# Kernel optimization log

Measured on AMD Instinct MI355X. Metric: run time of the kernel, lower is better.

Reference implementation:

```python
import jax, jax.numpy as jnp
import numpy as np

N_NODES = 50000
N_EDGES = 800000
N_GRAPHS = 64
IN_DIM, HID1, HID2, N_CLASSES = 128, 256, 128, 10


def setup_inputs() -> dict:
    key = jax.random.key(0)
    ks = jax.random.split(key, 12)
    x = jax.random.normal(ks[0], (N_NODES, IN_DIM), dtype=jnp.float32)
    src = jax.random.randint(ks[1], (N_EDGES,), 0, N_NODES, dtype=jnp.int32)
    dst = jax.random.randint(ks[2], (N_EDGES,), 0, N_NODES, dtype=jnp.int32)
    graph_id = jnp.sort(jax.random.randint(ks[3], (N_NODES,), 0, N_GRAPHS, dtype=jnp.int32))
    s1 = 1.0 / np.sqrt(IN_DIM)
    s2 = 1.0 / np.sqrt(HID1)
    s3 = 1.0 / np.sqrt(HID2)
    s4 = 1.0 / np.sqrt(12)
    return {
        'x': x, 'src': src, 'dst': dst, 'graph_id': graph_id,
        'W1': jax.random.normal(ks[4], (IN_DIM, HID1), dtype=jnp.float32) * s1,
        'b1': jnp.zeros((HID1,), dtype=jnp.float32),
        'W2': jax.random.normal(ks[5], (HID1, HID2), dtype=jnp.float32) * s2,
        'b2': jnp.zeros((HID2,), dtype=jnp.float32),
        'Wc1': jax.random.normal(ks[6], (HID2, 12), dtype=jnp.float32) * s3,
        'bc1': jnp.zeros((12,), dtype=jnp.float32),
        'Wc2': jax.random.normal(ks[7], (12, 12), dtype=jnp.float32) * s4,
        'bc2': jnp.zeros((12,), dtype=jnp.float32),
        'Wc3': jax.random.normal(ks[8], (12, N_CLASSES), dtype=jnp.float32) * s4,
        'bc3': jnp.zeros((N_CLASSES,), dtype=jnp.float32),
    }


def _graph_conv(x, W, b, src, dst, inv_sqrt_out, inv_sqrt_in, n_nodes):
    # DGL GraphConv, norm='both': D_out^{-1/2} applied to source feats,
    # sum-aggregate over edges, then D_in^{-1/2} on destination, then +bias.
    # Weight applied first (equivalent by linearity; reduces gather traffic
    # when out_dim < in_dim, and is exactly what DGL does in that case).
    xw = (x * inv_sqrt_out[:, None]) @ W                      # [N, out]
    agg = jax.ops.segment_sum(xw[src], dst, num_segments=n_nodes)  # SpMM
    return agg * inv_sqrt_in[:, None] + b


def reference(x, src, dst, graph_id, W1, b1, W2, b2, Wc1, bc1, Wc2, bc2, Wc3, bc3):
    n = x.shape[0]
    ones_e = jnp.ones(src.shape, dtype=x.dtype)
    deg_out = jnp.maximum(jax.ops.segment_sum(ones_e, src, num_segments=n), 1.0)
    deg_in = jnp.maximum(jax.ops.segment_sum(ones_e, dst, num_segments=n), 1.0)
    inv_o = jax.lax.rsqrt(deg_out)
    inv_i = jax.lax.rsqrt(deg_in)

    h = jax.nn.relu(_graph_conv(x, W1, b1, src, dst, inv_o, inv_i, n))
    h = jax.nn.relu(_graph_conv(h, W2, b2, src, dst, inv_o, inv_i, n))

    # dgl.mean_nodes: per-graph mean over nodes of the batched graph
    gsum = jax.ops.segment_sum(h, graph_id, num_segments=N_GRAPHS)   # [G, HID2]
    cnt = jnp.maximum(jax.ops.segment_sum(jnp.ones((n,), dtype=h.dtype), graph_id, num_segments=N_GRAPHS), 1.0)
    hg = gsum / cnt[:, None]

    # tiny 3-layer MLP (no activations in between, as in the source)
    out = hg @ Wc1 + bc1
    out = out @ Wc2 + bc2
    out = out @ Wc3 + bc3
    return out
```

## Files before the change

### kernel.cpp

```cpp
#include <hip/hip_runtime.h>
#include <hip/hip_bf16.h>

#define IN_DIM 128
#define HID1 256
#define HID2 128

#define HB_BINS 12500
#define HB_WORDS 6250
#define HB_CHUNKS 64
__global__ __launch_bounds__(256) void hist_src(const int* __restrict__ src,
                                                int E, int chunk_size,
                                                int* __restrict__ part, int N) {
    __shared__ int sm[HB_WORDS];
    const int base = blockIdx.y * HB_BINS;
    const int ebeg = blockIdx.x * chunk_size;
    const int eend = min(ebeg + chunk_size, E);
    for (int w = threadIdx.x; w < HB_WORDS; w += 256) sm[w] = 0;
    __syncthreads();
    for (int e = ebeg + threadIdx.x; e < eend; e += 256) {
        int v = src[e] - base;
        if ((unsigned)v < (unsigned)HB_BINS)
            atomicAdd(&sm[v >> 1], 1 << ((v & 1) * 16));
    }
    __syncthreads();
    const int nb = min(HB_BINS, N - base);
    int* dp = part + (size_t)blockIdx.x * N + base;
    for (int w = threadIdx.x; 2 * w < nb; w += 256) {
        int packed = sm[w];
        int b = 2 * w;
        dp[b] = packed & 0xffff;
        if (b + 1 < nb) dp[b + 1] = (packed >> 16) & 0xffff;
    }
}

__global__ __launch_bounds__(256) void hist_src_reduce(const int* __restrict__ part,
                                                       int N, float* __restrict__ inv_o) {
    int b = blockIdx.x * blockDim.x + threadIdx.x;
    if (b >= N) return;
    int d = 0;
#pragma unroll 4
    for (int k = 0; k < HB_CHUNKS; ++k) d += part[(size_t)k * N + b];
    inv_o[b] = rsqrtf((float)max(d, 1));
}

#define BK_SHIFT 8
#define NBUCK 196
#define NCHUNK 256
__global__ __launch_bounds__(256) void coarse_hist(const int* __restrict__ dst, int E,
                                                   int chunk_size, int* __restrict__ ccnt,
                                                   float* __restrict__ hg, int hg_n) {
    __shared__ int cnt[NBUCK];
    if (blockIdx.x == 0)
        for (int i = threadIdx.x; i < hg_n; i += 256) hg[i] = 0.f;
    for (int i = threadIdx.x; i < NBUCK; i += 256) cnt[i] = 0;
    __syncthreads();
    int ebeg = blockIdx.x * chunk_size, eend = min(ebeg + chunk_size, E);
    for (int e = ebeg + threadIdx.x; e < eend; e += 256)
        atomicAdd(&cnt[dst[e] >> BK_SHIFT], 1);
    __syncthreads();
    for (int i = threadIdx.x; i < NBUCK; i += 256) ccnt[blockIdx.x * NBUCK + i] = cnt[i];
}

__global__ __launch_bounds__(NCHUNK) void coarse_col(const int* __restrict__ ccnt,
                                                     int* __restrict__ coffpre,
                                                     int* __restrict__ ctot) {
    __shared__ int sm[NCHUNK];
    const int b = blockIdx.x, t = threadIdx.x;
    int v = ccnt[t * NBUCK + b];
    sm[t] = v;
    __syncthreads();
#pragma unroll
    for (int off = 1; off < NCHUNK; off <<= 1) {
        int u = (t >= off) ? sm[t - off] : 0;
        __syncthreads();
        sm[t] += u;
        __syncthreads();
    }
    coffpre[t * NBUCK + b] = sm[t] - v;
    if (t == NCHUNK - 1) ctot[b] = sm[t];
}

__device__ __forceinline__ void scan_bbase(const int* __restrict__ ctot, int* sm, int* bbase) {
    const int t = threadIdx.x;
    int v = (t < NBUCK) ? ctot[t] : 0;
    sm[t] = v;
    __syncthreads();
#pragma unroll
    for (int off = 1; off < 256; off <<= 1) {
        int u = (t >= off) ? sm[t - off] : 0;
        __syncthreads();
        sm[t] += u;
        __syncthreads();
    }
    if (t < NBUCK) bbase[t] = sm[t] - v;
    __syncthreads();
}

__global__ __launch_bounds__(256) void scat_a(const int* __restrict__ src,
                                              const int* __restrict__ dst, int E,
                                              int chunk_size,
                                              const int* __restrict__ coffpre,
                                              const int* __restrict__ ctot,
                                              int2* __restrict__ pairs) {
    __shared__ int sm[256];
    __shared__ int bbase[NBUCK];
    __shared__ int lcur[NBUCK];
    scan_bbase(ctot, sm, bbase);
    for (int i = threadIdx.x; i < NBUCK; i += 256)
        lcur[i] = bbase[i] + coffpre[blockIdx.x * NBUCK + i];
    __syncthreads();
    int ebeg = blockIdx.x * chunk_size, eend = min(ebeg + chunk_size, E);
    for (int e = ebeg + threadIdx.x; e < eend; e += 256) {
        int d = dst[e];
        int p = atomicAdd(&lcur[d >> BK_SHIFT], 1);
        pairs[p] = make_int2(src[e], d);
    }
}

__global__ __launch_bounds__(256) void scat_b(const int2* __restrict__ pairs,
                                              const int* __restrict__ ctot, int N,
                                              int* __restrict__ row,
                                              float* __restrict__ inv_i,
                                              int* __restrict__ csr_src) {
    __shared__ int sm[256];
    __shared__ int bbase[NBUCK];
    __shared__ int cnt[1 << BK_SHIFT];
    __shared__ int cur[1 << BK_SHIFT];
    const int b = blockIdx.x, t = threadIdx.x;
    scan_bbase(ctot, sm, bbase);
    const int segBase = bbase[b];
    const int segEnd = segBase + ctot[b];
    const int nb0 = b << BK_SHIFT;
    const int nbn = min(256, N - nb0);
    cnt[t] = 0;
    __syncthreads();
    for (int j = segBase + t; j < segEnd; j += 256)
        atomicAdd(&cnt[pairs[j].y - nb0], 1);
    __syncthreads();
    int v = cnt[t];
    sm[t] = v;
    __syncthreads();
#pragma unroll
    for (int off = 1; off < 256; off <<= 1) {
        int u = (t >= off) ? sm[t - off] : 0;
        __syncthreads();
        sm[t] += u;
        __syncthreads();
    }
    int excl = sm[t] - v;
    cur[t] = segBase + excl;
    if (t < nbn) {
        row[nb0 + t] = segBase + excl;
        inv_i[nb0 + t] = rsqrtf((float)max(v, 1));
        if (nb0 + t == N - 1) row[N] = segBase + excl + v;
    }
    __syncthreads();
    for (int j = segBase + t; j < segEnd; j += 256) {
        int2 pr = pairs[j];
        int p = atomicAdd(&cur[pr.y - nb0], 1);
        csr_src[p] = pr.x;
    }
}

__global__ void cvt_all(const float* __restrict__ x, const float* __restrict__ inv_o,
                        __hip_bfloat16* __restrict__ x_bf, int n4x,
                        const float* __restrict__ W1, __hip_bfloat16* __restrict__ W1t,
                        const float* __restrict__ W2, __hip_bfloat16* __restrict__ W2t) {
    const int S1 = IN_DIM * HID1;
    const int S2 = HID1 * HID2;
    int i = blockIdx.x * blockDim.x + threadIdx.x;
    if (i < n4x) {
        float s = inv_o[i >> 5];
        float4 v = reinterpret_cast<const float4*>(x)[i];
        __hip_bfloat16 b0 = __float2bfloat16(v.x * s);
        __hip_bfloat16 b1 = __float2bfloat16(v.y * s);
        __hip_bfloat16 b2 = __float2bfloat16(v.z * s);
        __hip_bfloat16 b3 = __float2bfloat16(v.w * s);
        ushort4 o = make_ushort4(*(unsigned short*)&b0, *(unsigned short*)&b1,
                                 *(unsigned short*)&b2, *(unsigned short*)&b3);
        reinterpret_cast<ushort4*>(x_bf)[i] = o;
    } else {
        int idx = i - n4x;
        if (idx < S1) {
            int k = idx / HID1, n = idx - k * HID1;
            W1t[n * IN_DIM + k] = __float2bfloat16(W1[idx]);
        } else if (idx < S1 + S2) {
            int j = idx - S1;
            int k = j / HID2, n = j - k * HID2;
            W2t[n * HID1 + k] = __float2bfloat16(W2[j]);
        }
    }
}

__device__ __forceinline__ void bf2_unpack(unsigned int p, float& lo, float& hi) {
    lo = __uint_as_float(p << 16);
    hi = __uint_as_float(p & 0xffff0000u);
}

__global__ __launch_bounds__(256) void spmm_kernel(const __hip_bfloat16* __restrict__ feat,
                                                   const int* __restrict__ row,
                                                   const int* __restrict__ csr_src,
                                                   __hip_bfloat16* __restrict__ out_bf, int N) {
    const int node = blockIdx.x * 4 + (threadIdx.x >> 6);
    if (node >= N) return;
    const int lane = threadIdx.x & 63;
    const unsigned int* fp = (const unsigned int*)feat;
    const int beg = row[node];
    const int end = row[node + 1];
    float a0 = 0.f, a1 = 0.f;
    int j = beg;
    for (; j + 8 <= end; j += 8) {
        int s0 = csr_src[j],     s1 = csr_src[j + 1], s2 = csr_src[j + 2], s3 = csr_src[j + 3];
        int s4 = csr_src[j + 4], s5 = csr_src[j + 5], s6 = csr_src[j + 6], s7 = csr_src[j + 7];
        unsigned int p0 = fp[(size_t)s0 * 64 + lane];
        unsigned int p1 = fp[(size_t)s1 * 64 + lane];
        unsigned int p2 = fp[(size_t)s2 * 64 + lane];
        unsigned int p3 = fp[(size_t)s3 * 64 + lane];
        unsigned int p4 = fp[(size_t)s4 * 64 + lane];
        unsigned int p5 = fp[(size_t)s5 * 64 + lane];
        unsigned int p6 = fp[(size_t)s6 * 64 + lane];
        unsigned int p7 = fp[(size_t)s7 * 64 + lane];
        float lo, hi;
        bf2_unpack(p0, lo, hi); a0 += lo; a1 += hi;
        bf2_unpack(p1, lo, hi); a0 += lo; a1 += hi;
        bf2_unpack(p2, lo, hi); a0 += lo; a1 += hi;
        bf2_unpack(p3, lo, hi); a0 += lo; a1 += hi;
        bf2_unpack(p4, lo, hi); a0 += lo; a1 += hi;
        bf2_unpack(p5, lo, hi); a0 += lo; a1 += hi;
        bf2_unpack(p6, lo, hi); a0 += lo; a1 += hi;
        bf2_unpack(p7, lo, hi); a0 += lo; a1 += hi;
    }
    for (; j + 4 <= end; j += 4) {
        int s0 = csr_src[j], s1 = csr_src[j + 1], s2 = csr_src[j + 2], s3 = csr_src[j + 3];
        unsigned int p0 = fp[(size_t)s0 * 64 + lane];
        unsigned int p1 = fp[(size_t)s1 * 64 + lane];
        unsigned int p2 = fp[(size_t)s2 * 64 + lane];
        unsigned int p3 = fp[(size_t)s3 * 64 + lane];
        float lo, hi;
        bf2_unpack(p0, lo, hi); a0 += lo; a1 += hi;
        bf2_unpack(p1, lo, hi); a0 += lo; a1 += hi;
        bf2_unpack(p2, lo, hi); a0 += lo; a1 += hi;
        bf2_unpack(p3, lo, hi); a0 += lo; a1 += hi;
    }
    for (; j < end; ++j) {
        unsigned int p0 = fp[(size_t)csr_src[j] * 64 + lane];
        float lo, hi;
        bf2_unpack(p0, lo, hi); a0 += lo; a1 += hi;
    }
    __hip_bfloat16 b0 = __float2bfloat16(a0);
    __hip_bfloat16 b1 = __float2bfloat16(a1);
    unsigned int packed = (unsigned int)(*(unsigned short*)&b0) |
                          ((unsigned int)(*(unsigned short*)&b1) << 16);
    ((unsigned int*)out_bf)[(size_t)node * 64 + lane] = packed;
}

#define SP_NODES 8
__global__ __launch_bounds__(256) void spmm_pool_kernel(const __hip_bfloat16* __restrict__ feat,
                                                        const int* __restrict__ row,
                                                        const int* __restrict__ csr_src,
                                                        const float* __restrict__ inv_i,
                                                        const float* __restrict__ b2,
                                                        const int* __restrict__ graph_id,
                                                        int N, float* __restrict__ hg_sum) {
    const int wave = blockIdx.x * 4 + (threadIdx.x >> 6);
    const int lane = threadIdx.x & 63;
    const int n0 = wave * SP_NODES;
    if (n0 >= N) return;
    const int n1 = min(n0 + SP_NODES, N);
    const unsigned int* fp = (const unsigned int*)feat;
    const float bias0 = b2[2 * lane];
    const float bias1 = b2[2 * lane + 1];
    int g = graph_id[n0];
    float p0s = 0.f, p1s = 0.f;
    for (int node = n0; node < n1; ++node) {
        int gi = graph_id[node];
        if (gi != g) {
            atomicAdd(&hg_sum[g * HID2 + 2 * lane], p0s);
            atomicAdd(&hg_sum[g * HID2 + 2 * lane + 1], p1s);
            p0s = p1s = 0.f;
            g = gi;
        }
        const int beg = row[node];
        const int end = row[node + 1];
        float a0 = 0.f, a1 = 0.f;
        int j = beg;
        for (; j + 4 <= end; j += 4) {
            int s0 = csr_src[j], s1 = csr_src[j + 1], s2 = csr_src[j + 2], s3 = csr_src[j + 3];
            unsigned int q0 = fp[(size_t)s0 * 64 + lane];
            unsigned int q1 = fp[(size_t)s1 * 64 + lane];
            unsigned int q2 = fp[(size_t)s2 * 64 + lane];
            unsigned int q3 = fp[(size_t)s3 * 64 + lane];
            float lo, hi;
            bf2_unpack(q0, lo, hi); a0 += lo; a1 += hi;
            bf2_unpack(q1, lo, hi); a0 += lo; a1 += hi;
            bf2_unpack(q2, lo, hi); a0 += lo; a1 += hi;
            bf2_unpack(q3, lo, hi); a0 += lo; a1 += hi;
        }
        for (; j < end; ++j) {
            unsigned int q0 = fp[(size_t)csr_src[j] * 64 + lane];
            float lo, hi;
            bf2_unpack(q0, lo, hi); a0 += lo; a1 += hi;
        }
        float ii = inv_i[node];
        p0s += fmaxf(a0 * ii + bias0, 0.f);
        p1s += fmaxf(a1 * ii + bias1, 0.f);
    }
    atomicAdd(&hg_sum[g * HID2 + 2 * lane], p0s);
    atomicAdd(&hg_sum[g * HID2 + 2 * lane + 1], p1s);
}

#define GBM 128
#define GBN 128
#define GBK 32
#define LPAD 40
typedef __attribute__((ext_vector_type(4))) float floatx4;
typedef __attribute__((ext_vector_type(8))) short shortx8;

__global__ __launch_bounds__(256) void mfma_gemm_kernel(const __hip_bfloat16* __restrict__ A,
                                                        const __hip_bfloat16* __restrict__ Bt,
                                                        __hip_bfloat16* __restrict__ C,
                                                        const float* __restrict__ scaleR,
                                                        const float* __restrict__ bias,
                                                        const float* __restrict__ scaleO,
                                                        int M, int Nn, int K, int doRelu) {
    __shared__ __align__(16) __hip_bfloat16 As[GBM * LPAD];
    __shared__ __align__(16) __hip_bfloat16 Bs[GBN * LPAD];
    const int tid = threadIdx.x;
    const int bm = blockIdx.x * GBM;
    const int bn = blockIdx.y * GBN;
    const int wid = tid >> 6;
    const int lane = tid & 63;
    const int wm = (wid & 1) * 64;
    const int wn = (wid >> 1) * 64;
    const int lrow = lane & 15;
    const int quad = lane >> 4;

    floatx4 acc[4][4] = {};

    for (int k0 = 0; k0 < K; k0 += GBK) {
#pragma unroll
        for (int it = 0; it < 2; ++it) {
            int slot = tid + (it << 8);
            int r = slot >> 2;
            int c = (slot & 3) << 3;
            int gr = bm + r;
            float4 v = make_float4(0.f, 0.f, 0.f, 0.f);
            if (gr < M) v = *reinterpret_cast<const float4*>(A + (size_t)gr * K + k0 + c);
            *reinterpret_cast<float4*>(&As[r * LPAD + c]) = v;
        }
#pragma unroll
        for (int it = 0; it < 2; ++it) {
            int slot = tid + (it << 8);
            int r = slot >> 2;
            int c = (slot & 3) << 3;
            float4 v = *reinterpret_cast<const float4*>(Bt + (size_t)(bn + r) * K + k0 + c);
            *reinterpret_cast<float4*>(&Bs[r * LPAD + c]) = v;
        }
        __syncthreads();

        shortx8 af[4], bf[4];
#pragma unroll
        for (int i = 0; i < 4; ++i)
            af[i] = *reinterpret_cast<const shortx8*>(&As[(wm + i * 16 + lrow) * LPAD + quad * 8]);
#pragma unroll
        for (int i = 0; i < 4; ++i)
            bf[i] = *reinterpret_cast<const shortx8*>(&Bs[(wn + i * 16 + lrow) * LPAD + quad * 8]);
#pragma unroll
        for (int im = 0; im < 4; ++im)
#pragma unroll
            for (int in = 0; in < 4; ++in)
                acc[im][in] = __builtin_amdgcn_mfma_f32_16x16x32_bf16(af[im], bf[in], acc[im][in], 0, 0, 0);
        __syncthreads();
    }

    float bv[4];
#pragma unroll
    for (int in = 0; in < 4; ++in)
        bv[in] = bias ? bias[bn + wn + in * 16 + lrow] : 0.f;

#pragma unroll
    for (int im = 0; im < 4; ++im) {
#pragma unroll
        for (int reg = 0; reg < 4; ++reg) {
            int r = bm + wm + im * 16 + quad * 4 + reg;
            if (r >= M) continue;
            float sR = scaleR ? scaleR[r] : 1.f;
            float sO = scaleO ? scaleO[r] : 1.f;
#pragma unroll
            for (int in = 0; in < 4; ++in) {
                int c = bn + wn + in * 16 + lrow;
                float v = acc[im][in][reg] * sR + bv[in];
                if (doRelu) v = fmaxf(v, 0.f);
                v *= sO;
                C[(size_t)r * Nn + c] = __float2bfloat16(v);
            }
        }
    }
}

__device__ __forceinline__ int lower_bound_i(const int* a, int n, int key) {
    int lo = 0, hi = n;
    while (lo < hi) {
        int mid = (lo + hi) >> 1;
        if (a[mid] < key) lo = mid + 1; else hi = mid;
    }
    return lo;
}

__global__ __launch_bounds__(64) void mlp_kernel(const float* __restrict__ hg_sum,
                                                 const int* __restrict__ graph_id, int n,
                                                 const float* __restrict__ Wc1, const float* __restrict__ bc1,
                                                 const float* __restrict__ Wc2, const float* __restrict__ bc2,
                                                 const float* __restrict__ Wc3, const float* __restrict__ bc3,
                                                 float* __restrict__ out) {
    const int g = blockIdx.x;
    const int t = threadIdx.x;
    __shared__ float h[HID2];
    __shared__ float t1[12];
    __shared__ float t2[12];
    __shared__ float s_inv_cnt;
    if (t == 0) {
        int beg = lower_bound_i(graph_id, n, g);
        int end = lower_bound_i(graph_id, n, g + 1);
        int c = end - beg;
        s_inv_cnt = 1.0f / (float)max(c, 1);
    }
    __syncthreads();
    const float ic = s_inv_cnt;
    for (int i = t; i < HID2; i += 64) h[i] = hg_sum[g * HID2 + i] * ic;
    __syncthreads();
    if (t < 12) {
        float a = bc1[t];
        for (int k = 0; k < HID2; ++k) a += h[k] * Wc1[k * 12 + t];
        t1[t] = a;
    }
    __syncthreads();
    if (t < 12) {
        float a = bc2[t];
        for (int k = 0; k < 12; ++k) a += t1[k] * Wc2[k * 12 + t];
        t2[t] = a;
    }
    __syncthreads();
    if (t < 10) {
        float a = bc3[t];
        for (int k = 0; k < 12; ++k) a += t2[k] * Wc3[k * 10 + t];
        out[g * 10 + t] = a;
    }
}

extern "C" void kernel_launch(void* const* d_in, const int* in_sizes, int n_in,
                              void* d_out, int out_size, void* d_ws, size_t ws_size,
                              hipStream_t stream) {
    const float* x        = (const float*)d_in[0];
    const int*   src      = (const int*)d_in[1];
    const int*   dst      = (const int*)d_in[2];
    const int*   graph_id = (const int*)d_in[3];
    const float* W1       = (const float*)d_in[4];
    const float* b1       = (const float*)d_in[5];
    const float* W2       = (const float*)d_in[6];
    const float* b2       = (const float*)d_in[7];
    const float* Wc1      = (const float*)d_in[8];
    const float* bc1      = (const float*)d_in[9];
    const float* Wc2      = (const float*)d_in[10];
    const float* bc2      = (const float*)d_in[11];
    const float* Wc3      = (const float*)d_in[12];
    const float* bc3      = (const float*)d_in[13];
    float* out = (float*)d_out;

    const int N = in_sizes[0] / IN_DIM;
    const int E = in_sizes[1];
    const int G = out_size / 10;

    char* ws = (char*)d_ws;
    size_t off = 0;
    auto alloc = [&](size_t bytes) -> char* {
        char* p = ws + off;
        off = (off + bytes + 255) & ~(size_t)255;
        return p;
    };
    float* inv_i   = (float*)alloc((size_t)N * 4);
    float* inv_o   = (float*)alloc((size_t)N * 4);
    int*   row     = (int*)alloc((size_t)(N + 1) * 4);
    int*   ccnt    = (int*)alloc((size_t)NCHUNK * NBUCK * 4);
    int*   coffpre = (int*)alloc((size_t)NCHUNK * NBUCK * 4);
    int*   ctot    = (int*)alloc((size_t)NBUCK * 4);
    int2*  pairs   = (int2*)alloc((size_t)E * 8);
    int*   csr_src = (int*)alloc((size_t)E * 4);
    float* hg      = (float*)alloc((size_t)G * HID2 * 4);
    __hip_bfloat16* x_bf    = (__hip_bfloat16*)alloc((size_t)N * IN_DIM * 2);
    __hip_bfloat16* W1t     = (__hip_bfloat16*)alloc((size_t)IN_DIM * HID1 * 2);
    __hip_bfloat16* W2t     = (__hip_bfloat16*)alloc((size_t)HID1 * HID2 * 2);
    __hip_bfloat16* agg1_bf = (__hip_bfloat16*)alloc((size_t)N * IN_DIM * 2);
    __hip_bfloat16* h1_bf   = (__hip_bfloat16*)alloc((size_t)N * HID1 * 2);
    __hip_bfloat16* xw2_bf  = (__hip_bfloat16*)alloc((size_t)N * HID2 * 2);

    int* part = (int*)h1_bf;

    const int hchunk = (E + HB_CHUNKS - 1) / HB_CHUNKS;
    const int n_ranges = (N + HB_BINS - 1) / HB_BINS;
    hist_src<<<dim3(HB_CHUNKS, n_ranges), 256, 0, stream>>>(src, E, hchunk, part, N);
    hist_src_reduce<<<(N + 255) / 256, 256, 0, stream>>>(part, N, inv_o);

    const int schunk = (E + NCHUNK - 1) / NCHUNK;
    coarse_hist<<<NCHUNK, 256, 0, stream>>>(dst, E, schunk, ccnt, hg, G * HID2);
    coarse_col<<<NBUCK, NCHUNK, 0, stream>>>(ccnt, coffpre, ctot);
    scat_a<<<NCHUNK, 256, 0, stream>>>(src, dst, E, schunk, coffpre, ctot, pairs);
    scat_b<<<NBUCK, 256, 0, stream>>>(pairs, ctot, N, row, inv_i, csr_src);

    const int n4x = N * IN_DIM / 4;
    cvt_all<<<(n4x + IN_DIM * HID1 + HID1 * HID2 + 255) / 256, 256, 0, stream>>>(
        x, inv_o, x_bf, n4x, W1, W1t, W2, W2t);

    spmm_kernel<<<(N + 3) / 4, 256, 0, stream>>>(x_bf, row, csr_src, agg1_bf, N);
    mfma_gemm_kernel<<<dim3((N + GBM - 1) / GBM, HID1 / GBN), 256, 0, stream>>>(
        agg1_bf, W1t, h1_bf, inv_i, b1, inv_o, N, HID1, IN_DIM, 1);

    mfma_gemm_kernel<<<dim3((N + GBM - 1) / GBM, HID2 / GBN), 256, 0, stream>>>(
        h1_bf, W2t, xw2_bf, nullptr, nullptr, nullptr, N, HID2, HID1, 0);
    const int npw = (N + SP_NODES - 1) / SP_NODES;
    spmm_pool_kernel<<<(npw + 3) / 4, 256, 0, stream>>>(xw2_bf, row, csr_src, inv_i, b2,
                                                        graph_id, N, hg);

    mlp_kernel<<<G, 64, 0, stream>>>(hg, graph_id, N, Wc1, bc1, Wc2, bc2, Wc3, bc3, out);
}
```

Measured before the change: 278.7 us.

## Gather SpMM rows with 16-byte loads split across four edge groups

```diff
diff --git a/kernel.cpp b/kernel.cpp
--- a/kernel.cpp
+++ b/kernel.cpp
@@ -197,6 +197,54 @@
     hi = __uint_as_float(p & 0xffff0000u);
 }
 
+__device__ __forceinline__ void acc_uint4(uint4 q, float* a) {
+    float lo, hi;
+    bf2_unpack(q.x, lo, hi); a[0] += lo; a[1] += hi;
+    bf2_unpack(q.y, lo, hi); a[2] += lo; a[3] += hi;
+    bf2_unpack(q.z, lo, hi); a[4] += lo; a[5] += hi;
+    bf2_unpack(q.w, lo, hi); a[6] += lo; a[7] += hi;
+}
+
+__device__ __forceinline__ unsigned int pack_bf2(float lo, float hi) {
+    __hip_bfloat16 b0 = __float2bfloat16(lo);
+    __hip_bfloat16 b1 = __float2bfloat16(hi);
+    return (unsigned int)(*(unsigned short*)&b0) |
+           ((unsigned int)(*(unsigned short*)&b1) << 16);
+}
+
+__device__ __forceinline__ void gather_node(const uint4* __restrict__ fp4,
+                                            const int* __restrict__ csr_src,
+                                            int beg, int end, int g, int c, float* a) {
+    int j = beg;
+    for (; j + 16 <= end; j += 16) {
+        int s0 = csr_src[j + g];
+        int s1 = csr_src[j + 4 + g];
+        int s2 = csr_src[j + 8 + g];
+        int s3 = csr_src[j + 12 + g];
+        uint4 q0 = fp4[(size_t)s0 * 16 + c];
+        uint4 q1 = fp4[(size_t)s1 * 16 + c];
+        uint4 q2 = fp4[(size_t)s2 * 16 + c];
+        uint4 q3 = fp4[(size_t)s3 * 16 + c];
+        acc_uint4(q0, a);
+        acc_uint4(q1, a);
+        acc_uint4(q2, a);
+        acc_uint4(q3, a);
+    }
+    for (; j + 4 <= end; j += 4) {
+        int s0 = csr_src[j + g];
+        uint4 q0 = fp4[(size_t)s0 * 16 + c];
+        acc_uint4(q0, a);
+    }
+    if (j < end) {
+        int e = j + g;
+        if (e < end) {
+            int s0 = csr_src[e];
+            uint4 q0 = fp4[(size_t)s0 * 16 + c];
+            acc_uint4(q0, a);
+        }
+    }
+}
+
 __global__ __launch_bounds__(256) void spmm_kernel(const __hip_bfloat16* __restrict__ feat,
                                                    const int* __restrict__ row,
                                                    const int* __restrict__ csr_src,
@@ -204,54 +252,26 @@
     const int node = blockIdx.x * 4 + (threadIdx.x >> 6);
     if (node >= N) return;
     const int lane = threadIdx.x & 63;
-    const unsigned int* fp = (const unsigned int*)feat;
+    const int g = lane >> 4;
+    const int c = lane & 15;
+    const uint4* fp4 = (const uint4*)feat;
     const int beg = row[node];
     const int end = row[node + 1];
-    float a0 = 0.f, a1 = 0.f;
-    int j = beg;
-    for (; j + 8 <= end; j += 8) {
-        int s0 = csr_src[j],     s1 = csr_src[j + 1], s2 = csr_src[j + 2], s3 = csr_src[j + 3];
-        int s4 = csr_src[j + 4], s5 = csr_src[j + 5], s6 = csr_src[j + 6], s7 = csr_src[j + 7];
-        unsigned int p0 = fp[(size_t)s0 * 64 + lane];
-        unsigned int p1 = fp[(size_t)s1 * 64 + lane];
-        unsigned int p2 = fp[(size_t)s2 * 64 + lane];
-        unsigned int p3 = fp[(size_t)s3 * 64 + lane];
-        unsigned int p4 = fp[(size_t)s4 * 64 + lane];
-        unsigned int p5 = fp[(size_t)s5 * 64 + lane];
-        unsigned int p6 = fp[(size_t)s6 * 64 + lane];
-        unsigned int p7 = fp[(size_t)s7 * 64 + lane];
-        float lo, hi;
-        bf2_unpack(p0, lo, hi); a0 += lo; a1 += hi;
-        bf2_unpack(p1, lo, hi); a0 += lo; a1 += hi;
-        bf2_unpack(p2, lo, hi); a0 += lo; a1 += hi;
-        bf2_unpack(p3, lo, hi); a0 += lo; a1 += hi;
-        bf2_unpack(p4, lo, hi); a0 += lo; a1 += hi;
-        bf2_unpack(p5, lo, hi); a0 += lo; a1 += hi;
-        bf2_unpack(p6, lo, hi); a0 += lo; a1 += hi;
-        bf2_unpack(p7, lo, hi); a0 += lo; a1 += hi;
-    }
-    for (; j + 4 <= end; j += 4) {
-        int s0 = csr_src[j], s1 = csr_src[j + 1], s2 = csr_src[j + 2], s3 = csr_src[j + 3];
-        unsigned int p0 = fp[(size_t)s0 * 64 + lane];
-        unsigned int p1 = fp[(size_t)s1 * 64 + lane];
-        unsigned int p2 = fp[(size_t)s2 * 64 + lane];
-        unsigned int p3 = fp[(size_t)s3 * 64 + lane];
-        float lo, hi;
-        bf2_unpack(p0, lo, hi); a0 += lo; a1 += hi;
-        bf2_unpack(p1, lo, hi); a0 += lo; a1 += hi;
-        bf2_unpack(p2, lo, hi); a0 += lo; a1 += hi;
-        bf2_unpack(p3, lo, hi); a0 += lo; a1 += hi;
-    }
-    for (; j < end; ++j) {
-        unsigned int p0 = fp[(size_t)csr_src[j] * 64 + lane];
-        float lo, hi;
-        bf2_unpack(p0, lo, hi); a0 += lo; a1 += hi;
-    }
-    __hip_bfloat16 b0 = __float2bfloat16(a0);
-    __hip_bfloat16 b1 = __float2bfloat16(a1);
-    unsigned int packed = (unsigned int)(*(unsigned short*)&b0) |
-                          ((unsigned int)(*(unsigned short*)&b1) << 16);
-    ((unsigned int*)out_bf)[(size_t)node * 64 + lane] = packed;
+    float a[8] = {};
+    gather_node(fp4, csr_src, beg, end, g, c, a);
+#pragma unroll
+    for (int i = 0; i < 8; ++i) {
+        a[i] += __shfl_xor(a[i], 16);
+        a[i] += __shfl_xor(a[i], 32);
+    }
+    if (lane < 16) {
+        uint4 o;
+        o.x = pack_bf2(a[0], a[1]);
+        o.y = pack_bf2(a[2], a[3]);
+        o.z = pack_bf2(a[4], a[5]);
+        o.w = pack_bf2(a[6], a[7]);
+        ((uint4*)out_bf)[(size_t)node * 16 + c] = o;
+    }
 }
 
 #define SP_NODES 8
@@ -264,49 +284,48 @@
                                                         int N, float* __restrict__ hg_sum) {
     const int wave = blockIdx.x * 4 + (threadIdx.x >> 6);
     const int lane = threadIdx.x & 63;
+    const int g4 = lane >> 4;
+    const int c = lane & 15;
     const int n0 = wave * SP_NODES;
     if (n0 >= N) return;
     const int n1 = min(n0 + SP_NODES, N);
-    const unsigned int* fp = (const unsigned int*)feat;
-    const float bias0 = b2[2 * lane];
-    const float bias1 = b2[2 * lane + 1];
+    const uint4* fp4 = (const uint4*)feat;
+    float4 bb0 = ((const float4*)b2)[c * 2];
+    float4 bb1 = ((const float4*)b2)[c * 2 + 1];
+    float bias[8] = {bb0.x, bb0.y, bb0.z, bb0.w, bb1.x, bb1.y, bb1.z, bb1.w};
     int g = graph_id[n0];
-    float p0s = 0.f, p1s = 0.f;
+    float p[8] = {};
     for (int node = n0; node < n1; ++node) {
         int gi = graph_id[node];
         if (gi != g) {
-            atomicAdd(&hg_sum[g * HID2 + 2 * lane], p0s);
-            atomicAdd(&hg_sum[g * HID2 + 2 * lane + 1], p1s);
-            p0s = p1s = 0.f;
+            if (lane < 16) {
+#pragma unroll
+                for (int i = 0; i < 8; ++i)
+                    atomicAdd(&hg_sum[g * HID2 + c * 8 + i], p[i]);
+            }
+#pragma unroll
+            for (int i = 0; i < 8; ++i) p[i] = 0.f;
             g = gi;
         }
         const int beg = row[node];
         const int end = row[node + 1];
-        float a0 = 0.f, a1 = 0.f;
-        int j = beg;
-        for (; j + 4 <= end; j += 4) {
-            int s0 = csr_src[j], s1 = csr_src[j + 1], s2 = csr_src[j + 2], s3 = csr_src[j + 3];
-            unsigned int q0 = fp[(size_t)s0 * 64 + lane];
-            unsigned int q1 = fp[(size_t)s1 * 64 + lane];
-            unsigned int q2 = fp[(size_t)s2 * 64 + lane];
-            unsigned int q3 = fp[(size_t)s3 * 64 + lane];
-            float lo, hi;
-            bf2_unpack(q0, lo, hi); a0 += lo; a1 += hi;
-            bf2_unpack(q1, lo, hi); a0 += lo; a1 += hi;
-            bf2_unpack(q2, lo, hi); a0 += lo; a1 += hi;
-            bf2_unpack(q3, lo, hi); a0 += lo; a1 += hi;
-        }
-        for (; j < end; ++j) {
-            unsigned int q0 = fp[(size_t)csr_src[j] * 64 + lane];
-            float lo, hi;
-            bf2_unpack(q0, lo, hi); a0 += lo; a1 += hi;
+        float a[8] = {};
+        gather_node(fp4, csr_src, beg, end, g4, c, a);
+#pragma unroll
+        for (int i = 0; i < 8; ++i) {
+            a[i] += __shfl_xor(a[i], 16);
+            a[i] += __shfl_xor(a[i], 32);
         }
         float ii = inv_i[node];
-        p0s += fmaxf(a0 * ii + bias0, 0.f);
-        p1s += fmaxf(a1 * ii + bias1, 0.f);
-    }
-    atomicAdd(&hg_sum[g * HID2 + 2 * lane], p0s);
-    atomicAdd(&hg_sum[g * HID2 + 2 * lane + 1], p1s);
+#pragma unroll
+        for (int i = 0; i < 8; ++i)
+            p[i] += fmaxf(a[i] * ii + bias[i], 0.f);
+    }
+    if (lane < 16) {
+#pragma unroll
+        for (int i = 0; i < 8; ++i)
+            atomicAdd(&hg_sum[g * HID2 + c * 8 + i], p[i]);
+    }
 }
 
 #define GBM 128
@@ -342,19 +361,19 @@
         for (int it = 0; it < 2; ++it) {
             int slot = tid + (it << 8);
             int r = slot >> 2;
-            int c = (slot & 3) << 3;
+            int cc = (slot & 3) << 3;
             int gr = bm + r;
             float4 v = make_float4(0.f, 0.f, 0.f, 0.f);
-            if (gr < M) v = *reinterpret_cast<const float4*>(A + (size_t)gr * K + k0 + c);
-            *reinterpret_cast<float4*>(&As[r * LPAD + c]) = v;
+            if (gr < M) v = *reinterpret_cast<const float4*>(A + (size_t)gr * K + k0 + cc);
+            *reinterpret_cast<float4*>(&As[r * LPAD + cc]) = v;
         }
 #pragma unroll
         for (int it = 0; it < 2; ++it) {
             int slot = tid + (it << 8);
             int r = slot >> 2;
-            int c = (slot & 3) << 3;
-            float4 v = *reinterpret_cast<const float4*>(Bt + (size_t)(bn + r) * K + k0 + c);
-            *reinterpret_cast<float4*>(&Bs[r * LPAD + c]) = v;
+            int cc = (slot & 3) << 3;
+            float4 v = *reinterpret_cast<const float4*>(Bt + (size_t)(bn + r) * K + k0 + cc);
+            *reinterpret_cast<float4*>(&Bs[r * LPAD + cc]) = v;
         }
         __syncthreads();
 
@@ -388,11 +407,11 @@
             float sO = scaleO ? scaleO[r] : 1.f;
 #pragma unroll
             for (int in = 0; in < 4; ++in) {
-                int c = bn + wn + in * 16 + lrow;
+                int cc = bn + wn + in * 16 + lrow;
                 float v = acc[im][in][reg] * sR + bv[in];
                 if (doRelu) v = fmaxf(v, 0.f);
                 v *= sO;
-                C[(size_t)r * Nn + c] = __float2bfloat16(v);
+                C[(size_t)r * Nn + cc] = __float2bfloat16(v);
             }
         }
     }
```

New measurement: 292.6 us. 5.0% more time.

## Pad CSR rows to multiples of eight with a zero dummy node

Applied to the files above, without the earlier changes.

```diff
diff --git a/kernel.cpp b/kernel.cpp
--- a/kernel.cpp
+++ b/kernel.cpp
@@ -46,6 +46,7 @@
 #define BK_SHIFT 8
 #define NBUCK 196
 #define NCHUNK 256
+#define PADCAP 2048
 __global__ __launch_bounds__(256) void coarse_hist(const int* __restrict__ dst, int E,
                                                    int chunk_size, int* __restrict__ ccnt,
                                                    float* __restrict__ hg, int hg_n) {
@@ -119,7 +120,8 @@
 
 __global__ __launch_bounds__(256) void scat_b(const int2* __restrict__ pairs,
                                               const int* __restrict__ ctot, int N,
-                                              int* __restrict__ row,
+                                              int* __restrict__ rowb,
+                                              int* __restrict__ rowe,
                                               float* __restrict__ inv_i,
                                               int* __restrict__ csr_src) {
     __shared__ int sm[256];
@@ -130,6 +132,7 @@
     scan_bbase(ctot, sm, bbase);
     const int segBase = bbase[b];
     const int segEnd = segBase + ctot[b];
+    const int pSegBase = bbase[b] + b * PADCAP;
     const int nb0 = b << BK_SHIFT;
     const int nbn = min(256, N - nb0);
     cnt[t] = 0;
@@ -138,7 +141,8 @@
         atomicAdd(&cnt[pairs[j].y - nb0], 1);
     __syncthreads();
     int v = cnt[t];
-    sm[t] = v;
+    int pv = (v + 7) & ~7;
+    sm[t] = pv;
     __syncthreads();
 #pragma unroll
     for (int off = 1; off < 256; off <<= 1) {
@@ -147,12 +151,14 @@
         sm[t] += u;
         __syncthreads();
     }
-    int excl = sm[t] - v;
-    cur[t] = segBase + excl;
+    int pexcl = sm[t] - pv;
+    int pbeg = pSegBase + pexcl;
+    cur[t] = pbeg;
     if (t < nbn) {
-        row[nb0 + t] = segBase + excl;
+        rowb[nb0 + t] = pbeg;
+        rowe[nb0 + t] = pbeg + pv;
         inv_i[nb0 + t] = rsqrtf((float)max(v, 1));
-        if (nb0 + t == N - 1) row[N] = segBase + excl + v;
+        for (int k = v; k < pv; ++k) csr_src[pbeg + k] = N;
     }
     __syncthreads();
     for (int j = segBase + t; j < segEnd; j += 256) {
@@ -164,6 +170,7 @@
 
 __global__ void cvt_all(const float* __restrict__ x, const float* __restrict__ inv_o,
                         __hip_bfloat16* __restrict__ x_bf, int n4x,
+                        __hip_bfloat16* __restrict__ xw2_bf, int N,
                         const float* __restrict__ W1, __hip_bfloat16* __restrict__ W1t,
                         const float* __restrict__ W2, __hip_bfloat16* __restrict__ W2t) {
     const int S1 = IN_DIM * HID1;
@@ -179,8 +186,12 @@
         ushort4 o = make_ushort4(*(unsigned short*)&b0, *(unsigned short*)&b1,
                                  *(unsigned short*)&b2, *(unsigned short*)&b3);
         reinterpret_cast<ushort4*>(x_bf)[i] = o;
+    } else if (i < n4x + 32) {
+        reinterpret_cast<ushort4*>(x_bf)[(size_t)N * 32 + (i - n4x)] = make_ushort4(0, 0, 0, 0);
+    } else if (i < n4x + 64) {
+        reinterpret_cast<ushort4*>(xw2_bf)[(size_t)N * 32 + (i - n4x - 32)] = make_ushort4(0, 0, 0, 0);
     } else {
-        int idx = i - n4x;
+        int idx = i - n4x - 64;
         if (idx < S1) {
             int k = idx / HID1, n = idx - k * HID1;
             W1t[n * IN_DIM + k] = __float2bfloat16(W1[idx]);
@@ -198,15 +209,16 @@
 }
 
 __global__ __launch_bounds__(256) void spmm_kernel(const __hip_bfloat16* __restrict__ feat,
-                                                   const int* __restrict__ row,
+                                                   const int* __restrict__ rowb,
+                                                   const int* __restrict__ rowe,
                                                    const int* __restrict__ csr_src,
                                                    __hip_bfloat16* __restrict__ out_bf, int N) {
     const int node = blockIdx.x * 4 + (threadIdx.x >> 6);
     if (node >= N) return;
     const int lane = threadIdx.x & 63;
     const unsigned int* fp = (const unsigned int*)feat;
-    const int beg = row[node];
-    const int end = row[node + 1];
+    const int beg = rowb[node];
+    const int end = rowe[node];
     float a0 = 0.f, a1 = 0.f;
     int j = beg;
     for (; j + 8 <= end; j += 8) {
@@ -230,18 +242,6 @@
         bf2_unpack(p6, lo, hi); a0 += lo; a1 += hi;
         bf2_unpack(p7, lo, hi); a0 += lo; a1 += hi;
     }
-    for (; j + 4 <= end; j += 4) {
-        int s0 = csr_src[j], s1 = csr_src[j + 1], s2 = csr_src[j + 2], s3 = csr_src[j + 3];
-        unsigned int p0 = fp[(size_t)s0 * 64 + lane];
-        unsigned int p1 = fp[(size_t)s1 * 64 + lane];
-        unsigned int p2 = fp[(size_t)s2 * 64 + lane];
-        unsigned int p3 = fp[(size_t)s3 * 64 + lane];
-        float lo, hi;
-        bf2_unpack(p0, lo, hi); a0 += lo; a1 += hi;
-        bf2_unpack(p1, lo, hi); a0 += lo; a1 += hi;
-        bf2_unpack(p2, lo, hi); a0 += lo; a1 += hi;
-        bf2_unpack(p3, lo, hi); a0 += lo; a1 += hi;
-    }
     for (; j < end; ++j) {
         unsigned int p0 = fp[(size_t)csr_src[j] * 64 + lane];
         float lo, hi;
@@ -254,9 +254,10 @@
     ((unsigned int*)out_bf)[(size_t)node * 64 + lane] = packed;
 }
 
-#define SP_NODES 8
+#define SP_NODES 4
 __global__ __launch_bounds__(256) void spmm_pool_kernel(const __hip_bfloat16* __restrict__ feat,
-                                                        const int* __restrict__ row,
+                                                        const int* __restrict__ rowb,
+                                                        const int* __restrict__ rowe,
                                                         const int* __restrict__ csr_src,
                                                         const float* __restrict__ inv_i,
                                                         const float* __restrict__ b2,
@@ -280,21 +281,30 @@
             p0s = p1s = 0.f;
             g = gi;
         }
-        const int beg = row[node];
-        const int end = row[node + 1];
+        const int beg = rowb[node];
+        const int end = rowe[node];
         float a0 = 0.f, a1 = 0.f;
         int j = beg;
-        for (; j + 4 <= end; j += 4) {
-            int s0 = csr_src[j], s1 = csr_src[j + 1], s2 = csr_src[j + 2], s3 = csr_src[j + 3];
+        for (; j + 8 <= end; j += 8) {
+            int s0 = csr_src[j],     s1 = csr_src[j + 1], s2 = csr_src[j + 2], s3 = csr_src[j + 3];
+            int s4 = csr_src[j + 4], s5 = csr_src[j + 5], s6 = csr_src[j + 6], s7 = csr_src[j + 7];
             unsigned int q0 = fp[(size_t)s0 * 64 + lane];
             unsigned int q1 = fp[(size_t)s1 * 64 + lane];
             unsigned int q2 = fp[(size_t)s2 * 64 + lane];
             unsigned int q3 = fp[(size_t)s3 * 64 + lane];
+            unsigned int q4 = fp[(size_t)s4 * 64 + lane];
+            unsigned int q5 = fp[(size_t)s5 * 64 + lane];
+            unsigned int q6 = fp[(size_t)s6 * 64 + lane];
+            unsigned int q7 = fp[(size_t)s7 * 64 + lane];
             float lo, hi;
             bf2_unpack(q0, lo, hi); a0 += lo; a1 += hi;
             bf2_unpack(q1, lo, hi); a0 += lo; a1 += hi;
             bf2_unpack(q2, lo, hi); a0 += lo; a1 += hi;
             bf2_unpack(q3, lo, hi); a0 += lo; a1 += hi;
+            bf2_unpack(q4, lo, hi); a0 += lo; a1 += hi;
+            bf2_unpack(q5, lo, hi); a0 += lo; a1 += hi;
+            bf2_unpack(q6, lo, hi); a0 += lo; a1 += hi;
+            bf2_unpack(q7, lo, hi); a0 += lo; a1 += hi;
         }
         for (; j < end; ++j) {
             unsigned int q0 = fp[(size_t)csr_src[j] * 64 + lane];
@@ -342,19 +352,19 @@
         for (int it = 0; it < 2; ++it) {
             int slot = tid + (it << 8);
             int r = slot >> 2;
-            int c = (slot & 3) << 3;
+            int cc = (slot & 3) << 3;
             int gr = bm + r;
             float4 v = make_float4(0.f, 0.f, 0.f, 0.f);
-            if (gr < M) v = *reinterpret_cast<const float4*>(A + (size_t)gr * K + k0 + c);
-            *reinterpret_cast<float4*>(&As[r * LPAD + c]) = v;
+            if (gr < M) v = *reinterpret_cast<const float4*>(A + (size_t)gr * K + k0 + cc);
+            *reinterpret_cast<float4*>(&As[r * LPAD + cc]) = v;
         }
 #pragma unroll
         for (int it = 0; it < 2; ++it) {
             int slot = tid + (it << 8);
             int r = slot >> 2;
-            int c = (slot & 3) << 3;
-            float4 v = *reinterpret_cast<const float4*>(Bt + (size_t)(bn + r) * K + k0 + c);
-            *reinterpret_cast<float4*>(&Bs[r * LPAD + c]) = v;
+            int cc = (slot & 3) << 3;
+            float4 v = *reinterpret_cast<const float4*>(Bt + (size_t)(bn + r) * K + k0 + cc);
+            *reinterpret_cast<float4*>(&Bs[r * LPAD + cc]) = v;
         }
         __syncthreads();
 
@@ -388,11 +398,11 @@
             float sO = scaleO ? scaleO[r] : 1.f;
 #pragma unroll
             for (int in = 0; in < 4; ++in) {
-                int c = bn + wn + in * 16 + lrow;
+                int cc = bn + wn + in * 16 + lrow;
                 float v = acc[im][in][reg] * sR + bv[in];
                 if (doRelu) v = fmaxf(v, 0.f);
                 v *= sO;
-                C[(size_t)r * Nn + c] = __float2bfloat16(v);
+                C[(size_t)r * Nn + cc] = __float2bfloat16(v);
             }
         }
     }
@@ -480,19 +490,20 @@
     };
     float* inv_i   = (float*)alloc((size_t)N * 4);
     float* inv_o   = (float*)alloc((size_t)N * 4);
-    int*   row     = (int*)alloc((size_t)(N + 1) * 4);
+    int*   rowb    = (int*)alloc((size_t)N * 4);
+    int*   rowe    = (int*)alloc((size_t)N * 4);
     int*   ccnt    = (int*)alloc((size_t)NCHUNK * NBUCK * 4);
     int*   coffpre = (int*)alloc((size_t)NCHUNK * NBUCK * 4);
     int*   ctot    = (int*)alloc((size_t)NBUCK * 4);
     int2*  pairs   = (int2*)alloc((size_t)E * 8);
-    int*   csr_src = (int*)alloc((size_t)E * 4);
+    int*   csr_src = (int*)alloc(((size_t)E + (size_t)NBUCK * PADCAP) * 4);
     float* hg      = (float*)alloc((size_t)G * HID2 * 4);
-    __hip_bfloat16* x_bf    = (__hip_bfloat16*)alloc((size_t)N * IN_DIM * 2);
+    __hip_bfloat16* x_bf    = (__hip_bfloat16*)alloc((size_t)(N + 1) * IN_DIM * 2);
     __hip_bfloat16* W1t     = (__hip_bfloat16*)alloc((size_t)IN_DIM * HID1 * 2);
     __hip_bfloat16* W2t     = (__hip_bfloat16*)alloc((size_t)HID1 * HID2 * 2);
     __hip_bfloat16* agg1_bf = (__hip_bfloat16*)alloc((size_t)N * IN_DIM * 2);
     __hip_bfloat16* h1_bf   = (__hip_bfloat16*)alloc((size_t)N * HID1 * 2);
-    __hip_bfloat16* xw2_bf  = (__hip_bfloat16*)alloc((size_t)N * HID2 * 2);
+    __hip_bfloat16* xw2_bf  = (__hip_bfloat16*)alloc((size_t)(N + 1) * HID2 * 2);
 
     int* part = (int*)h1_bf;
 
@@ -505,20 +516,20 @@
     coarse_hist<<<NCHUNK, 256, 0, stream>>>(dst, E, schunk, ccnt, hg, G * HID2);
     coarse_col<<<NBUCK, NCHUNK, 0, stream>>>(ccnt, coffpre, ctot);
     scat_a<<<NCHUNK, 256, 0, stream>>>(src, dst, E, schunk, coffpre, ctot, pairs);
-    scat_b<<<NBUCK, 256, 0, stream>>>(pairs, ctot, N, row, inv_i, csr_src);
+    scat_b<<<NBUCK, 256, 0, stream>>>(pairs, ctot, N, rowb, rowe, inv_i, csr_src);
 
     const int n4x = N * IN_DIM / 4;
-    cvt_all<<<(n4x + IN_DIM * HID1 + HID1 * HID2 + 255) / 256, 256, 0, stream>>>(
-        x, inv_o, x_bf, n4x, W1, W1t, W2, W2t);
-
-    spmm_kernel<<<(N + 3) / 4, 256, 0, stream>>>(x_bf, row, csr_src, agg1_bf, N);
+    cvt_all<<<(n4x + 64 + IN_DIM * HID1 + HID1 * HID2 + 255) / 256, 256, 0, stream>>>(
+        x, inv_o, x_bf, n4x, xw2_bf, N, W1, W1t, W2, W2t);
+
+    spmm_kernel<<<(N + 3) / 4, 256, 0, stream>>>(x_bf, rowb, rowe, csr_src, agg1_bf, N);
     mfma_gemm_kernel<<<dim3((N + GBM - 1) / GBM, HID1 / GBN), 256, 0, stream>>>(
         agg1_bf, W1t, h1_bf, inv_i, b1, inv_o, N, HID1, IN_DIM, 1);
 
     mfma_gemm_kernel<<<dim3((N + GBM - 1) / GBM, HID2 / GBN), 256, 0, stream>>>(
         h1_bf, W2t, xw2_bf, nullptr, nullptr, nullptr, N, HID2, HID1, 0);
     const int npw = (N + SP_NODES - 1) / SP_NODES;
-    spmm_pool_kernel<<<(npw + 3) / 4, 256, 0, stream>>>(xw2_bf, row, csr_src, inv_i, b2,
+    spmm_pool_kernel<<<(npw + 3) / 4, 256, 0, stream>>>(xw2_bf, rowb, rowe, csr_src, inv_i, b2,
                                                         graph_id, N, hg);
 
     mlp_kernel<<<G, 64, 0, stream>>>(hg, graph_id, N, Wc1, bc1, Wc2, bc2, Wc3, bc3, out);
```

Result: no change. 277.9 us (-0.3%).
